# Kernel optimization log

Measured on AMD Instinct MI355X. Metric: run time of the kernel, lower is better.

The kernel has to match this reference:

```python
import jax, jax.numpy as jnp
import numpy as np

DIM = 512; H = 8; KH = 2; G = 4; DH = 64        # dim, q heads, kv heads, GQA group, head dim
BALL = 128; SEL = 64; TOPK = 2; PDIM = 3        # sliding ball, compress/selection block, topk, pos dim
SCALE = DH ** -0.5


def _rms_norm(x, gamma):
    return x * jax.lax.rsqrt(jnp.mean(x * x, axis=-1, keepdims=True) + 1e-6) * gamma


def _rotary(t):
    # t: (B, h, S, DH); GPT-NeoX style rotate-half rotary embedding
    S = t.shape[-2]
    inv = 1.0 / (10000.0 ** (jnp.arange(0, DH, 2, dtype=jnp.float32) / DH))
    f = jnp.arange(S, dtype=jnp.float32)[:, None] * inv          # (S, DH/2)
    cos = jnp.concatenate([jnp.cos(f), jnp.cos(f)], -1)
    sin = jnp.concatenate([jnp.sin(f), jnp.sin(f)], -1)
    t1, t2 = jnp.split(t, 2, -1)
    return t * cos + jnp.concatenate([-t2, t1], -1) * sin


def _forward(x, pos, pe_w, pe_b, gamma, wq, wk, wv, k_pos, v_pos,
             k_w1, k_b1, k_w2, k_b2, v_w1, v_b1, v_w2, v_b2,
             mem_k, mem_v, w_combine, w_out, num_batches):
    B = num_batches
    # relative position of leaves wrt ball center (no-grad in original)
    p = jax.lax.stop_gradient(pos).reshape(-1, SEL, PDIM)
    rel = (p - p.mean(axis=1, keepdims=True)).reshape(-1, PDIM)
    x = x + rel @ pe_w + pe_b
    x = x.reshape(B, -1, DIM)
    S = x.shape[1]
    nb = S // SEL
    h = _rms_norm(x, gamma)
    q = (h @ wq).reshape(B, S, H, DH).transpose(0, 2, 1, 3)      # (B,H,S,DH)
    k = (h @ wk).reshape(B, S, KH, DH).transpose(0, 2, 1, 3)     # (B,KH,S,DH)
    v = (h @ wv).reshape(B, S, KH, DH).transpose(0, 2, 1, 3)
    qr, kr = _rotary(q), _rotary(k)

    # --- compressed branch: per-block intra-pos emb + MLP compression ---
    kb = k.reshape(B, KH, nb, SEL, DH) + k_pos[None, :, None]
    vb = v.reshape(B, KH, nb, SEL, DH) + v_pos[None, :, None]
    ck = jax.nn.relu(kb.reshape(B, KH, nb, SEL * DH) @ k_w1 + k_b1) @ k_w2 + k_b2
    cv = jax.nn.relu(vb.reshape(B, KH, nb, SEL * DH) @ v_w1 + v_b1) @ v_w2 + v_b2
    ck = jnp.concatenate([jnp.broadcast_to(mem_k[None], (B, KH, 1, DH)), ck], axis=2)
    cv = jnp.concatenate([jnp.broadcast_to(mem_v[None], (B, KH, 1, DH)), cv], axis=2)
    qg = qr.reshape(B, KH, G, S, DH)
    csim = jnp.einsum('bkgsd,bknd->bkgsn', qg, ck) * SCALE
    cattn = jax.nn.softmax(csim, axis=-1)
    cout = jnp.einsum('bkgsn,bknd->bkgsd', cattn, cv).reshape(B, H, S, DH)

    # --- top-k block selection from compressed attention importance ---
    imp = cattn[..., 1:].mean(axis=2)                            # share over grouped q heads: (B,KH,S,nb)
    imp_blk = imp.reshape(B, KH, nb, SEL, nb).mean(axis=3)       # per query block: (B,KH,nb,nb)
    _, sel = jax.lax.top_k(imp_blk, TOPK)                        # (B,KH,nb,TOPK)

    # --- fine branch: each query block attends own + TOPK selected blocks ---
    kblk = kr.reshape(B, KH, nb, SEL, DH)
    vblk = v.reshape(B, KH, nb, SEL, DH)
    gather = jax.vmap(jax.vmap(lambda t, s: t[s]))               # (nb,SEL,DH),(nb,TOPK)->(nb,TOPK,SEL,DH)
    fk = jnp.concatenate([gather(kblk, sel), kblk[:, :, :, None]], axis=3)
    fv = jnp.concatenate([gather(vblk, sel), vblk[:, :, :, None]], axis=3)
    fk = fk.reshape(B, KH, nb, (TOPK + 1) * SEL, DH)
    fv = fv.reshape(B, KH, nb, (TOPK + 1) * SEL, DH)
    qb = qr.reshape(B, KH, G, nb, SEL, DH)
    fsim = jnp.einsum('bkgnqd,bknmd->bkgnqm', qb, fk) * SCALE
    fout = jnp.einsum('bkgnqm,bknmd->bkgnqd', jax.nn.softmax(fsim, -1), fv)
    fout = fout.reshape(B, H, S, DH)

    # --- sliding branch: MiniBallAttn = plain SDPA within balls of size 128 ---
    nw = S // BALL
    qw = qr.reshape(B, H, nw, BALL, DH)
    kw = jnp.repeat(kr, G, axis=1).reshape(B, H, nw, BALL, DH)
    vw = jnp.repeat(v, G, axis=1).reshape(B, H, nw, BALL, DH)
    ssim = jnp.einsum('bhnqd,bhnkd->bhnqk', qw, kw) * SCALE
    sout = jnp.einsum('bhnqk,bhnkd->bhnqd', jax.nn.softmax(ssim, -1), vw)
    sout = sout.reshape(B, H, S, DH)

    # --- sigmoid-gated strategy combine, merge heads, out projection ---
    gates = jax.nn.sigmoid(h @ w_combine).reshape(B, S, H, 3).transpose(0, 2, 1, 3)
    out = gates[..., 0:1] * cout + gates[..., 1:2] * fout + gates[..., 2:3] * sout
    out = out.transpose(0, 2, 1, 3).reshape(B, S, H * DH) @ w_out
    return out.reshape(-1, DIM)


def setup_inputs() -> dict:
    key = jax.random.key(0)
    ks = jax.random.split(key, 16)
    Bn, S = 8, 4096
    N = Bn * S
    CD = SEL * DH
    def lin(k, fi, fo):
        return (jax.random.normal(k, (fi, fo), jnp.float32) / np.sqrt(fi)).astype(jnp.float32)
    return {
        'x': jax.random.normal(ks[0], (N, DIM), jnp.float32),
        'pos': jax.random.normal(ks[1], (N, PDIM), jnp.float32),
        'pe_w': lin(ks[2], PDIM, DIM),
        'pe_b': jnp.zeros((DIM,), jnp.float32),
        'gamma': jnp.ones((DIM,), jnp.float32),
        'wq': lin(ks[3], DIM, H * DH),
        'wk': lin(ks[4], DIM, KH * DH),
        'wv': lin(ks[5], DIM, KH * DH),
        'k_pos': jax.random.normal(ks[6], (KH, SEL, DH), jnp.float32) * 0.02,
        'v_pos': jax.random.normal(ks[7], (KH, SEL, DH), jnp.float32) * 0.02,
        'k_w1': lin(ks[8], CD, CD), 'k_b1': jnp.zeros((CD,), jnp.float32),
        'k_w2': lin(ks[9], CD, DH), 'k_b2': jnp.zeros((DH,), jnp.float32),
        'v_w1': lin(ks[10], CD, CD), 'v_b1': jnp.zeros((CD,), jnp.float32),
        'v_w2': lin(ks[11], CD, DH), 'v_b2': jnp.zeros((DH,), jnp.float32),
        'mem_k': jax.random.normal(ks[12], (KH, 1, DH), jnp.float32) * 0.02,
        'mem_v': jax.random.normal(ks[13], (KH, 1, DH), jnp.float32) * 0.02,
        'w_combine': lin(ks[14], DIM, 3 * H),
        'w_out': lin(ks[15], H * DH, DIM),
        'num_batches': 8,
    }


def reference(x, pos, pe_w, pe_b, gamma, wq, wk, wv, k_pos, v_pos,
              k_w1, k_b1, k_w2, k_b2, v_w1, v_b1, v_w2, v_b2,
              mem_k, mem_v, w_combine, w_out, num_batches):
    return _forward(x, pos, pe_w, pe_b, gamma, wq, wk, wv, k_pos, v_pos,
                    k_w1, k_b1, k_w2, k_b2, v_w1, v_b1, v_w2, v_b2,
                    mem_k, mem_v, w_combine, w_out, num_batches)
```

## Files before the change

kernel.cpp:

```cpp
#include <hip/hip_runtime.h>
#include <stdint.h>

#define DEVI static __device__ __forceinline__
typedef unsigned short u16;
typedef __bf16 bhalf8 __attribute__((ext_vector_type(8)));
typedef float f32x4 __attribute__((ext_vector_type(4)));

DEVI u16 f2bf(float f) {
  union { float f; unsigned u; } v; v.f = f;
  unsigned r = v.u + 0x7FFFu + ((v.u >> 16) & 1u);
  return (u16)(r >> 16);
}
DEVI float bf2f(u16 h) {
  union { unsigned u; float f; } v; v.u = ((unsigned)h) << 16;
  return v.f;
}
DEVI f32x4 MFMA(bhalf8 a, bhalf8 b, f32x4 c) {
  return __builtin_amdgcn_mfma_f32_16x16x32_bf16(a, b, c, 0, 0, 0);
}
DEVI bhalf8 LD8(const u16* p) { return *(const bhalf8*)p; }
DEVI f32x4 zero4() { f32x4 z = {0.f, 0.f, 0.f, 0.f}; return z; }

#define GLDS16(gp, lp) __builtin_amdgcn_global_load_lds( \
    (const __attribute__((address_space(1))) void*)(gp), \
// ... 40 lines not shown
  if (bidx < 1792) {
    int idx = bidx * 256 + threadIdx.x;
    int k = idx & 511, n = idx >> 9;
    float v;
    if (n < 512) v = wq[(size_t)k*512 + n];
    else if (n < 640) v = wk[(size_t)k*128 + n - 512];
    else if (n < 768) v = wv[(size_t)k*128 + n - 640];
    else if (n < 792) v = wc[(size_t)k*24 + n - 768];
    else v = 0.f;
    u16 h = f2bf(v); hi[idx] = h; lo[idx] = f2bf(v - bf2f(h));
  } else {
    int idx = (bidx - 1792) * 256 + threadIdx.x;
    int s = idx >> 5, i = idx & 31;
    float e = (float)(2*i) * (1.0f/64.0f);
    float inv = 1.0f / powf(10000.0f, e);
    float f = (float)s * inv;
    ct[idx] = cosf(f); st[idx] = sinf(f);
  }
}

__global__ __launch_bounds__(256) void nsa_vT16(const u16* __restrict__ v16, u16* __restrict__ vT) {
  int blk = blockIdx.x;
  int st = (blk & 63) * 64, bkh = blk >> 6;
  __shared__ u16 tile[64][72];
  int t = threadIdx.x;
  int s = t >> 2, c0 = (t & 3) * 16;
  const u16* src = v16 + ((size_t)bkh*4096 + st + s) * 64;
  *(int4*)&tile[s][c0]   = *(const int4*)&src[c0];
  *(int4*)&tile[s][c0+8] = *(const int4*)&src[c0+8];
  __syncthreads();
  int d = t >> 2, s0 = (t & 3) * 16;
  u16* dst = vT + ((size_t)bkh*64 + d)*4096 + st + s0;
#pragma unroll
  for (int j = 0; j < 16; ++j) dst[j] = tile[s0+j][d];
}

__global__ __launch_bounds__(256) void nsa_wT(const float* __restrict__ src, u16* __restrict__ dhi,
    u16* __restrict__ dlo, int K, int N) {
  __shared__ float tile[64][65];
  int k0 = blockIdx.x * 64, n0 = blockIdx.y * 64;
  int t = threadIdx.x, r = t >> 2, c0 = (t & 3) * 16;
#pragma unroll
  for (int j = 0; j < 16; ++j) tile[r][c0+j] = src[(size_t)(k0+r)*N + n0 + c0 + j];
  __syncthreads();
  size_t ob = (size_t)(n0 + r)*K + k0 + c0;
#pragma unroll
  for (int j = 0; j < 16; ++j) {
    float v = tile[c0+j][r];
    u16 h = f2bf(v); dhi[ob+j] = h;
    if (dlo) dlo[ob+j] = f2bf(v - bf2f(h));
  }
}

__global__ __launch_bounds__(256) void nsa_init_c(const float* __restrict__ mem, const float* __restrict__ b2,
    float* __restrict__ c32) {
  int idx = blockIdx.x * 256 + threadIdx.x;
  if (idx >= 81920) return;
  int d = idx & 63, n = (idx >> 6) % 80, kh = (idx / (80*64)) & 1;
  c32[idx] = (n == 0) ? mem[kh*64 + d] : ((n <= 64) ? b2[d] : 0.f);
}

__global__ __launch_bounds__(256) void nsa_red64(const float* __restrict__ part, float* __restrict__ c32) {
  int idx = blockIdx.x * 256 + threadIdx.x;
  int m = idx >> 6, d = idx & 63;
  float s = 0.f;
#pragma unroll
  for (int kc = 0; kc < 8; ++kc) s += part[((size_t)kc*1024 + m)*64 + d];
  int bkh = m >> 6, n = m & 63;
  c32[(((size_t)bkh)*80 + 1 + n)*64 + d] += s;
}

template<bool SPLIT>
__global__ __launch_bounds__(256) void nsa_mlp_fuse(const float* __restrict__ part,
    const float* __restrict__ bias, u16* __restrict__ oh, u16* __restrict__ ol) {
  size_t i = ((size_t)blockIdx.x * 256 + threadIdx.x) * 4;
  int c = (int)(i & 4095);
  float4 a = *(const float4*)&part[i];
  float4 b = *(const float4*)&part[(size_t)4194304 + i];
  float v0 = fmaxf(a.x + b.x + bias[c+0], 0.f);
  float v1 = fmaxf(a.y + b.y + bias[c+1], 0.f);
  float v2 = fmaxf(a.z + b.z + bias[c+2], 0.f);
  float v3 = fmaxf(a.w + b.w + bias[c+3], 0.f);
  u16 h0 = f2bf(v0), h1 = f2bf(v1), h2 = f2bf(v2), h3 = f2bf(v3);
  ((unsigned long long*)oh)[i >> 2] = (unsigned long long)h0 | ((unsigned long long)h1 << 16) |
                                      ((unsigned long long)h2 << 32) | ((unsigned long long)h3 << 48);
  if (SPLIT) {
    u16 l0 = f2bf(v0 - bf2f(h0)), l1 = f2bf(v1 - bf2f(h1));
    u16 l2 = f2bf(v2 - bf2f(h2)), l3 = f2bf(v3 - bf2f(h3));
    ((unsigned long long*)ol)[i >> 2] = (unsigned long long)l0 | ((unsigned long long)l1 << 16) |
                                        ((unsigned long long)l2 << 32) | ((unsigned long long)l3 << 48);
  }
}

__global__ __launch_bounds__(256) void nsa_ckcv(const float* __restrict__ ck32, const float* __restrict__ cv32,
    u16* __restrict__ ckh, u16* __restrict__ ckl, u16* __restrict__ cvT) {
  int idx = blockIdx.x * 256 + threadIdx.x;
  if (idx < 81920) {
    float v = ck32[idx];
    u16 h = f2bf(v); ckh[idx] = h; ckl[idx] = f2bf(v - bf2f(h));
  } else if (idx < 81920 + 8*2*64*96) {
    int j = idx - 81920;
    int cc = j % 96, d = (j / 96) & 63, bkh = j / (96*64);
    float v = (cc < 80) ? cv32[((size_t)bkh*80 + cc)*64 + d] : 0.f;
    cvT[j] = f2bf(v);
  }
}

__global__ __launch_bounds__(256) void nsa_sentinel(float* __restrict__ o, int n, float val) {
  int i = blockIdx.x * 256 + threadIdx.x;
  if (i < n) o[i] = val;
}

template<bool SPLIT, int EPI>
__global__ __launch_bounds__(256) void nsa_gemm(const u16* __restrict__ Ah, const u16* __restrict__ Al,
    const u16* __restrict__ Bh, const u16* __restrict__ Bl, int K, int N,
    const float* __restrict__ p_cos, float* __restrict__ p_sin,
    u16* __restrict__ out_hi, u16* __restrict__ out_lo, float* __restrict__ og,
    const float* __restrict__ kpos, const float* __restrict__ vpos,
    u16* __restrict__ krb, u16* __restrict__ kbh, u16* __restrict__ kbl,
    u16* __restrict__ v16o, u16* __restrict__ vbh) {
  constexpr int NB = SPLIT ? 4 : 2;
  __shared__ u16 sm[NB * 2 * 4096];
  const int t = threadIdx.x, w = t >> 6, l = t & 63;
  const int wm = w >> 1, wn = w & 1;
  int m0, n0;
  if constexpr (EPI == 0) {
    const int bid = blockIdx.y * 256 + blockIdx.x;
    const int xcd = bid & 7, j = bid >> 3;
    const int mg = j / 56, rem = j % 56;
    const int nn = rem >> 3, mi = rem & 7;
    m0 = ((xcd * 4 + mg) * 8 + mi) * 128;
    n0 = nn * 128;
  } else {
    const int MBn = gridDim.x;
    const int nwg = MBn * gridDim.y;
    const int bid = blockIdx.y * MBn + blockIdx.x;
    const int swz = (bid & 7) * (nwg >> 3) + (bid >> 3);
    m0 = (swz % MBn) * 128; n0 = (swz / MBn) * 128;
  }
  const int klen = K / (int)gridDim.z;
  const int kb0 = blockIdx.z * klen;
  const int row = l & 15;
  const int kc8 = ((l >> 4) ^ ((l >> 1) & 3)) * 8;
  const int gsc = ((l & 3) ^ ((l >> 3) & 3)) * 8;
  const int sr = l >> 2;
  f32x4 acc[4][4];
#pragma unroll
  for (int a = 0; a < 4; ++a)
#pragma unroll
    for (int b = 0; b < 4; ++b) acc[a][b] = zero4();

  auto STAGE = [&](int buf, int k0) {
    u16* base = sm + buf * NB * 4096;
#pragma unroll
    for (int s2 = 0; s2 < 2; ++s2) {
      int seg = w*2 + s2;
      int r = seg*16 + sr;
      size_t ga = (size_t)(m0 + r)*K + k0 + gsc;
      size_t gb = (size_t)(n0 + r)*K + k0 + gsc;
      GLDS16(&Ah[ga], base + seg*512);
      GLDS16(&Bh[gb], base + 4096 + seg*512);
      if (SPLIT) {
        GLDS16(&Al[ga], base + 2*4096 + seg*512);
        GLDS16(&Bl[gb], base + 3*4096 + seg*512);
      }
    }
  };

  const int nt = klen >> 5;
  STAGE(0, kb0);
  __syncthreads();
  int cur = 0;
  for (int kt = 0; kt < nt; ++kt) {
    if (kt + 1 < nt) STAGE(cur ^ 1, kb0 + (kt + 1) * 32);
    u16* bA  = sm + cur * NB * 4096;
    u16* bB  = bA + 4096;
    u16* bAl = bA + 2*4096;
    u16* bBl = bA + 3*4096;
    bhalf8 af[4], afl[4];
#pragma unroll
    for (int mf = 0; mf < 4; ++mf) {
      af[mf] = LD8(&bA[(wm*64 + mf*16 + row)*32 + kc8]);
      if (SPLIT) afl[mf] = LD8(&bAl[(wm*64 + mf*16 + row)*32 + kc8]);
    }
#pragma unroll
// ... 96 lines not shown
#pragma unroll
    for (int mf = 0; mf < 4; ++mf)
#pragma unroll
      for (int nf = 0; nf < 4; ++nf)
#pragma unroll
        for (int i = 0; i < 4; ++i) {
          int r = m0 + wm*64 + mf*16 + (l >> 4)*4 + i;
          int c = n0 + wn*64 + nf*16 + (l & 15);
          p_sin[(size_t)r*N + c] = acc[mf][nf][i];
        }
  } else {
    const int M = (int)gridDim.x * 128;
#pragma unroll
    for (int mf = 0; mf < 4; ++mf)
#pragma unroll
      for (int nf = 0; nf < 4; ++nf)
#pragma unroll
        for (int i = 0; i < 4; ++i) {
          int r = m0 + wm*64 + mf*16 + (l >> 4)*4 + i;
          int c = n0 + wn*64 + nf*16 + (l & 15);
          p_sin[((size_t)blockIdx.z * M + r) * (size_t)N + c] = acc[mf][nf][i];
        }
  }
}

template<bool SPLIT>
__global__ __launch_bounds__(256) void nsa_gemm64(const u16* __restrict__ Ah, const u16* __restrict__ Al,
    const u16* __restrict__ Bh, const u16* __restrict__ Bl, float* __restrict__ part) {
  constexpr int NB = SPLIT ? 4 : 2;
  __shared__ u16 sm[NB * 2 * 2048];
  const int t = threadIdx.x, w = t >> 6, l = t & 63;
  const int mt = blockIdx.x, kc = blockIdx.y;
  const int row = l & 15;
  const int kc8 = ((l >> 4) ^ ((l >> 1) & 3)) * 8;
  const int gsc = ((l & 3) ^ ((l >> 3) & 3)) * 8;
  const int sr = l >> 2;
  f32x4 acc[4];
#pragma unroll
  for (int a = 0; a < 4; ++a) acc[a] = zero4();

  auto STAGE = [&](int buf, int k0) {
    u16* base = sm + buf * NB * 2048;
    int r = w*16 + sr;
    size_t ga = (size_t)(mt*64 + r)*4096 + k0 + gsc;
    size_t gb = (size_t)r*4096 + k0 + gsc;
    GLDS16(&Ah[ga], base + w*512);
    GLDS16(&Bh[gb], base + 2048 + w*512);
    if (SPLIT) {
      GLDS16(&Al[ga], base + 2*2048 + w*512);
      GLDS16(&Bl[gb], base + 3*2048 + w*512);
    }
  };

  STAGE(0, kc*512);
  __syncthreads();
  int cur = 0;
  for (int kt = 0; kt < 16; ++kt) {
    if (kt + 1 < 16) STAGE(cur ^ 1, kc*512 + (kt + 1) * 32);
    u16* bA  = sm + cur * NB * 2048;
    u16* bB  = bA + 2048;
    u16* bAl = bA + 2*2048;
    u16* bBl = bA + 3*2048;
    bhalf8 a = LD8(&bA[(w*16 + row)*32 + kc8]);
    bhalf8 al;
    if (SPLIT) al = LD8(&bAl[(w*16 + row)*32 + kc8]);
#pragma unroll
    for (int nf = 0; nf < 4; ++nf) {
      bhalf8 b = LD8(&bB[(nf*16 + row)*32 + kc8]);
      bhalf8 bl;
      if (SPLIT) bl = LD8(&bBl[(nf*16 + row)*32 + kc8]);
      acc[nf] = MFMA(a, b, acc[nf]);
      if (SPLIT) {
        acc[nf] = MFMA(a, bl, acc[nf]);
        acc[nf] = MFMA(al, b, acc[nf]);
      }
    }
    __syncthreads();
    cur ^= 1;
  }
#pragma unroll
  for (int nf = 0; nf < 4; ++nf)
#pragma unroll
    for (int i = 0; i < 4; ++i) {
      int m = mt*64 + w*16 + (l >> 4)*4 + i;
      int d = nf*16 + (l & 15);
      part[((size_t)kc*1024 + m)*64 + d] = acc[nf][i];
    }
}


__global__ __launch_bounds__(256) void nsa_attn_comp(const u16* __restrict__ qrh, const u16* __restrict__ qrl,
    const u16* __restrict__ ckh, const u16* __restrict__ ckl, const u16* __restrict__ cvT,
    const float* __restrict__ g32, u16* __restrict__ comb, float* __restrict__ imp) {
  __shared__ u16 smem[27392];
  __shared__ float sImp[4 * 80];
  u16* sKh = smem;
  u16* sKl = smem + 5760;
  u16* sVT = smem + 11520;
  u16* sQh = smem + 18176;
  u16* sQl = smem + 22784;
  u16* sP  = smem + 18176;
  const int t = threadIdx.x, w = t >> 6, l = t & 63;
  const int bid = blockIdx.x;
  const int qt = bid & 63, kh = (bid >> 6) & 1, b = bid >> 7;
  const int row = l & 15, kg = (l >> 4) * 8;
  size_t kbase = (size_t)(b*2 + kh) * 80 * 64;
  size_t vbase = (size_t)(b*2 + kh) * 64 * 96;
  for (int e = t; e < 640; e += 256) {
    int r = e >> 3, c = (e & 7) * 8;
    *(int4*)&sKh[r*72 + c] = *(const int4*)&ckh[kbase + r*64 + c];
    *(int4*)&sKl[r*72 + c] = *(const int4*)&ckl[kbase + r*64 + c];
  }
  for (int e = t; e < 768; e += 256) {
    int r = e / 12, ch = e % 12;
    *(int4*)&sVT[r*104 + ch*8] = *(const int4*)&cvT[vbase + (size_t)r*96 + ch*8];
  }
  float accImp = 0.f;
  for (int g = 0; g < 4; ++g) {
    if (g) __syncthreads();
    size_t qbase = ((size_t)((b*2 + kh)*4 + g)*4096 + qt*64) * 64;
    for (int e = t; e < 512; e += 256) {
      int r = e >> 3, c = (e & 7) * 8;
      *(int4*)&sQh[r*72 + c] = *(const int4*)&qrh[qbase + r*64 + c];
      *(int4*)&sQl[r*72 + c] = *(const int4*)&qrl[qbase + r*64 + c];
    }
    __syncthreads();
    f32x4 sc[5];
#pragma unroll
    for (int nf = 0; nf < 5; ++nf) sc[nf] = zero4();
#pragma unroll
    for (int kk = 0; kk < 2; ++kk) {
      bhalf8 ah = LD8(&sQh[(w*16 + row)*72 + kk*32 + kg]);
      bhalf8 al = LD8(&sQl[(w*16 + row)*72 + kk*32 + kg]);
#pragma unroll
      for (int nf = 0; nf < 5; ++nf) {
        bhalf8 bh = LD8(&sKh[(nf*16 + row)*72 + kk*32 + kg]);
        bhalf8 bl = LD8(&sKl[(nf*16 + row)*72 + kk*32 + kg]);
        sc[nf] = MFMA(ah, bh, sc[nf]);
        sc[nf] = MFMA(ah, bl, sc[nf]);
        sc[nf] = MFMA(al, bh, sc[nf]);
      }
    }
    float mx[4] = {-1e30f, -1e30f, -1e30f, -1e30f};
#pragma unroll
    for (int nf = 0; nf < 5; ++nf)
#pragma unroll
      for (int i = 0; i < 4; ++i) {
        int col = nf*16 + (l & 15);
        float v = (col < 65) ? sc[nf][i] * 0.125f : -1e30f;
        sc[nf][i] = v;
        mx[i] = fmaxf(mx[i], v);
      }
#pragma unroll
    for (int i = 0; i < 4; ++i)
#pragma unroll
      for (int o = 1; o < 16; o <<= 1) mx[i] = fmaxf(mx[i], __shfl_xor(mx[i], o));
    float sum[4] = {0.f, 0.f, 0.f, 0.f};
#pragma unroll
    for (int nf = 0; nf < 5; ++nf)
#pragma unroll
      for (int i = 0; i < 4; ++i) {
        int col = nf*16 + (l & 15);
        float p = (col < 65) ? expf(sc[nf][i] - mx[i]) : 0.f;
        sc[nf][i] = p;
        sum[i] += p;
      }
#pragma unroll
    for (int i = 0; i < 4; ++i)
#pragma unroll
      for (int o = 1; o < 16; o <<= 1) sum[i] += __shfl_xor(sum[i], o);
    float inv[4];
#pragma unroll
    for (int i = 0; i < 4; ++i) inv[i] = 1.0f / sum[i];
    __syncthreads();
#pragma unroll
    for (int nf = 0; nf < 5; ++nf)
#pragma unroll
      for (int i = 0; i < 4; ++i)
        sP[(w*16 + (l >> 4)*4 + i)*104 + nf*16 + (l & 15)] = f2bf(sc[nf][i] * inv[i]);
#pragma unroll
    for (int i = 0; i < 4; ++i)
      sP[(w*16 + (l >> 4)*4 + i)*104 + 80 + (l & 15)] = 0;
#pragma unroll
    for (int nf = 0; nf < 5; ++nf) {
      float cs = 0.f;
#pragma unroll
      for (int i = 0; i < 4; ++i) cs += sc[nf][i] * inv[i];
      cs += __shfl_xor(cs, 16);
      cs += __shfl_xor(cs, 32);
      if (l < 16) sImp[w*80 + nf*16 + l] = cs;
    }
    __syncthreads();
    if (t < 64) {
      int n = t + 1;
      accImp += sImp[n] + sImp[80 + n] + sImp[160 + n] + sImp[240 + n];
    }
    f32x4 ov[4];
#pragma unroll
    for (int nf = 0; nf < 4; ++nf) ov[nf] = zero4();
#pragma unroll
    for (int kk = 0; kk < 3; ++kk) {
      bhalf8 a = LD8(&sP[(w*16 + row)*104 + kk*32 + kg]);
#pragma unroll
      for (int nf = 0; nf < 4; ++nf) {
        bhalf8 bv = LD8(&sVT[(nf*16 + row)*104 + kk*32 + kg]);
        ov[nf] = MFMA(a, bv, ov[nf]);
      }
    }
    int hq = kh*4 + g;
#pragma unroll
    for (int i = 0; i < 4; ++i) {
      int q = qt*64 + w*16 + (l >> 4)*4 + i;
      float gate = g32[((size_t)b*4096 + q)*24 + hq*3 + 0];
#pragma unroll
      for (int nf = 0; nf < 4; ++nf) {
        int d = nf*16 + (l & 15);
        comb[(((size_t)b*4096 + q)*8 + hq)*64 + d] = f2bf(gate * ov[nf][i]);
      }
    }
  }
  if (t < 64) imp[(size_t)bid*64 + t] = accImp * (1.0f/256.0f);
}

__global__ __launch_bounds__(64) void nsa_top2(const float* __restrict__ imp, int* __restrict__ sel) {
  int blk = blockIdx.x;
  int l = threadIdx.x;
  float v = imp[(size_t)blk*64 + l];
  float v1 = v; int i1 = l;
#pragma unroll
  for (int o = 1; o < 64; o <<= 1) {
    float ovv = __shfl_xor(v1, o); int oi = __shfl_xor(i1, o);
    if (ovv > v1 || (ovv == v1 && oi < i1)) { v1 = ovv; i1 = oi; }
  }
  float v2 = (l == i1) ? -3.0e38f : v; int i2 = l;
#pragma unroll
  for (int o = 1; o < 64; o <<= 1) {
    float ovv = __shfl_xor(v2, o); int oi = __shfl_xor(i2, o);
    if (ovv > v2 || (ovv == v2 && oi < i2)) { v2 = ovv; i2 = oi; }
  }
  if (l == 0) { sel[blk*2 + 0] = i1; sel[blk*2 + 1] = i2; }
}

__global__ __launch_bounds__(256) void nsa_attn_fine(const u16* __restrict__ qrh, const u16* __restrict__ kr,
    const u16* __restrict__ vT, const int* __restrict__ sel, const float* __restrict__ g32,
    u16* __restrict__ comb) {
  __shared__ u16 smem[31232];
  u16* sK  = smem;
  u16* sP  = smem;
  u16* sVT = smem + 13824;
  u16* sQ  = smem + 26624;
  const int t = threadIdx.x, w = t >> 6, l = t & 63;
  const int bid = blockIdx.x;
  const int qt = bid & 63, kh = (bid >> 6) & 1, b = bid >> 7;
  const int row = l & 15, kg = (l >> 4) * 8;
  const int s0 = sel[bid*2 + 0] & 63, s1 = sel[bid*2 + 1] & 63;
  size_t kvb = (size_t)(b*2 + kh) * 4096 * 64;
  size_t vtb = (size_t)(b*2 + kh) * 64 * 4096;
  for (int e = t; e < 1536; e += 256) {
    int r = e / 24, ch = e % 24;
    int n0 = ch * 8, bi = n0 >> 6;
    int blkid = (bi == 0) ? s0 : ((bi == 1) ? s1 : qt);
    int sidx = blkid*64 + (n0 & 63);
    *(int4*)&sVT[r*200 + n0] = *(const int4*)&vT[vtb + (size_t)r*4096 + sidx];
  }
  for (int g = 0; g < 4; ++g) {
    __syncthreads();
    for (int e = t; e < 1536; e += 256) {
      int r = e >> 3, c = (e & 7) * 8;
      int bi = r >> 6;
      int blkid = (bi == 0) ? s0 : ((bi == 1) ? s1 : qt);
      int sidx = blkid*64 + (r & 63);
      *(int4*)&sK[r*72 + c] = *(const int4*)&kr[kvb + (size_t)sidx*64 + c];
    }
    size_t qbase = ((size_t)((b*2 + kh)*4 + g)*4096 + qt*64) * 64;
    for (int e = t; e < 512; e += 256) {
      int r = e >> 3, c = (e & 7) * 8;
      *(int4*)&sQ[r*72 + c] = *(const int4*)&qrh[qbase + r*64 + c];
    }
    __syncthreads();
    f32x4 sc[12];
#pragma unroll
    for (int nf = 0; nf < 12; ++nf) sc[nf] = zero4();
#pragma unroll
    for (int kk = 0; kk < 2; ++kk) {
      bhalf8 a = LD8(&sQ[(w*16 + row)*72 + kk*32 + kg]);
#pragma unroll
      for (int nf = 0; nf < 12; ++nf) {
        bhalf8 bk = LD8(&sK[(nf*16 + row)*72 + kk*32 + kg]);
        sc[nf] = MFMA(a, bk, sc[nf]);
      }
    }
    float mx[4] = {-1e30f, -1e30f, -1e30f, -1e30f};
#pragma unroll
    for (int nf = 0; nf < 12; ++nf)
#pragma unroll
      for (int i = 0; i < 4; ++i) {
        float v = sc[nf][i] * 0.125f;
        sc[nf][i] = v;
        mx[i] = fmaxf(mx[i], v);
      }
#pragma unroll
    for (int i = 0; i < 4; ++i)
#pragma unroll
      for (int o = 1; o < 16; o <<= 1) mx[i] = fmaxf(mx[i], __shfl_xor(mx[i], o));
    float sum[4] = {0.f, 0.f, 0.f, 0.f};
#pragma unroll
    for (int nf = 0; nf < 12; ++nf)
#pragma unroll
      for (int i = 0; i < 4; ++i) {
        float p = expf(sc[nf][i] - mx[i]);
        sc[nf][i] = p;
        sum[i] += p;
      }
#pragma unroll
    for (int i = 0; i < 4; ++i)
#pragma unroll
      for (int o = 1; o < 16; o <<= 1) sum[i] += __shfl_xor(sum[i], o);
    float inv[4];
#pragma unroll
    for (int i = 0; i < 4; ++i) inv[i] = 1.0f / sum[i];
    __syncthreads();
#pragma unroll
    for (int nf = 0; nf < 12; ++nf)
#pragma unroll
      for (int i = 0; i < 4; ++i)
        sP[(w*16 + (l >> 4)*4 + i)*200 + nf*16 + (l & 15)] = f2bf(sc[nf][i] * inv[i]);
    __syncthreads();
    f32x4 ovv[4];
#pragma unroll
    for (int nf = 0; nf < 4; ++nf) ovv[nf] = zero4();
#pragma unroll
    for (int kk = 0; kk < 6; ++kk) {
      bhalf8 a = LD8(&sP[(w*16 + row)*200 + kk*32 + kg]);
#pragma unroll
      for (int nf = 0; nf < 4; ++nf) {
        bhalf8 bv = LD8(&sVT[(nf*16 + row)*200 + kk*32 + kg]);
        ovv[nf] = MFMA(a, bv, ovv[nf]);
      }
    }
    int hq = kh*4 + g;
#pragma unroll
    for (int i = 0; i < 4; ++i) {
      int q = qt*64 + w*16 + (l >> 4)*4 + i;
      float gate = g32[((size_t)b*4096 + q)*24 + hq*3 + 1];
#pragma unroll
      for (int nf = 0; nf < 4; ++nf) {
        int d = nf*16 + (l & 15);
        size_t oi = (((size_t)b*4096 + q)*8 + hq)*64 + d;
        comb[oi] = f2bf(bf2f(comb[oi]) + gate * ovv[nf][i]);
      }
    }
  }
}

__global__ __launch_bounds__(256) void nsa_attn_slide(const u16* __restrict__ qrh, const u16* __restrict__ kr,
    const u16* __restrict__ vT, const float* __restrict__ g32, u16* __restrict__ comb) {
  __shared__ u16 smem[31232];
  u16* sK  = smem;
  u16* sVT = smem + 9216;
  u16* sQ  = smem + 17920;
  u16* sP  = smem + 22528;
  const int t = threadIdx.x, w = t >> 6, l = t & 63;
  const int bid = blockIdx.x;
  const int ball = bid & 31, kh = (bid >> 5) & 1, b = bid >> 6;
  const int row = l & 15, kg = (l >> 4) * 8;
  const int ks0 = ball * 128;
  size_t kvb = (size_t)(b*2 + kh) * 4096 * 64;
  size_t vtb = (size_t)(b*2 + kh) * 64 * 4096;
  for (int e = t; e < 1024; e += 256) {
    int r = e >> 3, c = (e & 7) * 8;
    *(int4*)&sK[r*72 + c] = *(const int4*)&kr[kvb + (size_t)(ks0 + r)*64 + c];
  }
  for (int e = t; e < 1024; e += 256) {
    int r = e >> 4, ch = e & 15;
    *(int4*)&sVT[r*136 + ch*8] = *(const int4*)&vT[vtb + (size_t)r*4096 + ks0 + ch*8];
  }
  for (int hq = 0; hq < 4; ++hq) {
    int hh = kh*4 + hq;
    for (int qh = 0; qh < 2; ++qh) {
      int qt = ball*2 + qh;
      __syncthreads();
      size_t qbase = ((size_t)(b*8 + hh)*4096 + qt*64) * 64;
      for (int e = t; e < 512; e += 256) {
        int r = e >> 3, c = (e & 7) * 8;
        *(int4*)&sQ[r*72 + c] = *(const int4*)&qrh[qbase + r*64 + c];
      }
      __syncthreads();
      f32x4 sc[8];
#pragma unroll
      for (int nf = 0; nf < 8; ++nf) sc[nf] = zero4();
#pragma unroll
      for (int kk = 0; kk < 2; ++kk) {
        bhalf8 a = LD8(&sQ[(w*16 + row)*72 + kk*32 + kg]);
#pragma unroll
        for (int nf = 0; nf < 8; ++nf) {
          bhalf8 bk = LD8(&sK[(nf*16 + row)*72 + kk*32 + kg]);
          sc[nf] = MFMA(a, bk, sc[nf]);
        }
      }
      float mx[4] = {-1e30f, -1e30f, -1e30f, -1e30f};
#pragma unroll
      for (int nf = 0; nf < 8; ++nf)
#pragma unroll
        for (int i = 0; i < 4; ++i) {
          float v = sc[nf][i] * 0.125f;
          sc[nf][i] = v;
          mx[i] = fmaxf(mx[i], v);
        }
#pragma unroll
      for (int i = 0; i < 4; ++i)
#pragma unroll
        for (int o = 1; o < 16; o <<= 1) mx[i] = fmaxf(mx[i], __shfl_xor(mx[i], o));
      float sum[4] = {0.f, 0.f, 0.f, 0.f};
#pragma unroll
      for (int nf = 0; nf < 8; ++nf)
#pragma unroll
        for (int i = 0; i < 4; ++i) {
          float p = expf(sc[nf][i] - mx[i]);
          sc[nf][i] = p;
          sum[i] += p;
        }
#pragma unroll
      for (int i = 0; i < 4; ++i)
#pragma unroll
        for (int o = 1; o < 16; o <<= 1) sum[i] += __shfl_xor(sum[i], o);
      float inv[4];
#pragma unroll
      for (int i = 0; i < 4; ++i) inv[i] = 1.0f / sum[i];
#pragma unroll
      for (int nf = 0; nf < 8; ++nf)
#pragma unroll
        for (int i = 0; i < 4; ++i)
          sP[(w*16 + (l >> 4)*4 + i)*136 + nf*16 + (l & 15)] = f2bf(sc[nf][i] * inv[i]);
      f32x4 ovv[4];
#pragma unroll
      for (int nf = 0; nf < 4; ++nf) ovv[nf] = zero4();
#pragma unroll
      for (int kk = 0; kk < 4; ++kk) {
        bhalf8 a = LD8(&sP[(w*16 + row)*136 + kk*32 + kg]);
#pragma unroll
        for (int nf = 0; nf < 4; ++nf) {
          bhalf8 bv = LD8(&sVT[(nf*16 + row)*136 + kk*32 + kg]);
          ovv[nf] = MFMA(a, bv, ovv[nf]);
        }
      }
#pragma unroll
// ... 1 lines not shown
        int q = qt*64 + w*16 + (l >> 4)*4 + i;
        float gate = g32[((size_t)b*4096 + q)*24 + hh*3 + 2];
#pragma unroll
        for (int nf = 0; nf < 4; ++nf) {
          int d = nf*16 + (l & 15);
          size_t oi = (((size_t)b*4096 + q)*8 + hh)*64 + d;
          comb[oi] = f2bf(bf2f(comb[oi]) + gate * ovv[nf][i]);
        }
      }
    }
  }
}


extern "C" void kernel_launch(void* const* d_in, const int* in_sizes, int n_in,
                              void* d_out, int out_size, void* d_ws, size_t ws_size,
                              hipStream_t stream) {
  const float* x     = (const float*)d_in[0];
  const float* pos   = (const float*)d_in[1];
  const float* pe_w  = (const float*)d_in[2];
  const float* pe_b  = (const float*)d_in[3];
  const float* gamma = (const float*)d_in[4];
  const float* wq    = (const float*)d_in[5];
  const float* wk    = (const float*)d_in[6];
  const float* wv    = (const float*)d_in[7];
  const float* k_pos = (const float*)d_in[8];
  const float* v_pos = (const float*)d_in[9];
  const float* k_w1  = (const float*)d_in[10];
  const float* k_b1  = (const float*)d_in[11];
  const float* k_w2  = (const float*)d_in[12];
  const float* k_b2  = (const float*)d_in[13];
  const float* v_w1  = (const float*)d_in[14];
  const float* v_b1  = (const float*)d_in[15];
  const float* v_w2  = (const float*)d_in[16];
  const float* v_b2  = (const float*)d_in[17];
  const float* mem_k = (const float*)d_in[18];
  const float* mem_v = (const float*)d_in[19];
  const float* w_cmb = (const float*)d_in[20];
  const float* w_out = (const float*)d_in[21];
  float* out = (float*)d_out;
  char* ws = (char*)d_ws;

  size_t off = 0;
  auto A = [&](size_t b) { size_t o = off; off += (b + 255) & ~(size_t)255; return o; };
  const size_t oR1 = A(67108864);
  const size_t oR2 = A(67108864);
  const size_t oR4 = A(16777216);
  const size_t oR5 = A(16777216);
  const size_t oR6 = A(16777216);
  const size_t oR7 = A(16777216);
  const size_t oR8 = A(3145728);
  const size_t oR9 = A(2097152);
  const size_t o_cos = A(524288),  o_sin = A(524288);
  const size_t o_ck32 = A(327680), o_cv32 = A(327680);
  const size_t o_ckh = A(163840),  o_ckl = A(163840);
  const size_t o_cvT = A(196608);
  const size_t o_woh = A(524288),  o_wol = A(524288);
  const size_t o_imp = A(262144);
  const size_t o_sel = A(8192);
  const size_t o_part = A(2097152);
  const size_t o_part1 = A(33554432);

  if (ws_size < off) {
    nsa_sentinel<<<(out_size + 255)/256, 256, 0, stream>>>(out, out_size, (float)(ws_size >> 20));
    return;
  }

#define WP(T, o) ((T*)(ws + (o)))
  u16*  h_hi = WP(u16, oR1);           u16* h_lo = WP(u16, oR1 + 33554432);
  u16*  w1h  = WP(u16, oR1);           u16* w1l  = WP(u16, oR1 + 33554432);
  u16*  combp = WP(u16, oR1);
  u16*  qrh  = WP(u16, oR2);           u16* qrl  = WP(u16, oR2 + 33554432);
  u16*  th   = WP(u16, oR4);           u16* tl   = WP(u16, oR4 + 8388608);
  u16*  v16b = WP(u16, oR5);           u16* vbh  = WP(u16, oR5 + 8388608);
  u16*  kbh  = WP(u16, oR6);           u16* kbl  = WP(u16, oR6 + 8388608);
  u16*  krb  = WP(u16, oR7);           u16* vTb  = WP(u16, oR7 + 8388608);
  float* g32 = WP(float, oR8);
  u16*  wch  = WP(u16, oR9);           u16* wcl  = WP(u16, oR9 + 917504);
  u16*  w2h  = WP(u16, oR9);           u16* w2l  = WP(u16, oR9 + 524288);
  u16*  w2vh = WP(u16, oR9 + 1048576); u16* w2vl = WP(u16, oR9 + 1572864);
  float* cosb = WP(float, o_cos);      float* sinb = WP(float, o_sin);
  float* ck32 = WP(float, o_ck32);     float* cv32 = WP(float, o_cv32);
  u16*  ckh  = WP(u16, o_ckh);         u16* ckl  = WP(u16, o_ckl);
  u16*  cvT  = WP(u16, o_cvT);
  u16*  woh  = WP(u16, o_woh);         u16* wol  = WP(u16, o_wol);
  float* imp = WP(float, o_imp);
  int*  selp = WP(int, o_sel);
  float* part = WP(float, o_part);
  float* part1 = WP(float, o_part1);

  nsa_hnorm<<<32768, 256, 0, stream>>>(x, pos, pe_w, pe_b, gamma, h_hi, h_lo);
  nsa_wcat_rope<<<2304, 256, 0, stream>>>(wq, wk, wv, w_cmb, wch, wcl, cosb, sinb);
  nsa_gemm<true, 0><<<dim3(256, 7, 1), 256, 0, stream>>>(h_hi, h_lo, wch, wcl, 512, 896,
      cosb, sinb, qrh, qrl, g32, k_pos, v_pos, krb, kbh, kbl, v16b, vbh);
  nsa_vT16<<<1024, 256, 0, stream>>>(v16b, vTb);
  nsa_wT<<<dim3(64, 64), 256, 0, stream>>>(k_w1, w1h, w1l, 4096, 4096);
  nsa_gemm<true, 3><<<dim3(8, 32, 2), 256, 0, stream>>>(kbh, kbl, w1h, w1l, 4096, 4096,
      nullptr, part1, nullptr, nullptr, nullptr, nullptr, nullptr, nullptr, nullptr, nullptr,
      nullptr, nullptr);
  nsa_mlp_fuse<true><<<4096, 256, 0, stream>>>(part1, k_b1, th, tl);
  nsa_wT<<<dim3(64, 1), 256, 0, stream>>>(k_w2, w2h, w2l, 4096, 64);
  nsa_init_c<<<320, 256, 0, stream>>>(mem_k, k_b2, ck32);
  nsa_gemm64<true><<<dim3(16, 8), 256, 0, stream>>>(th, tl, w2h, w2l, part);
  nsa_red64<<<256, 256, 0, stream>>>(part, ck32);
  nsa_wT<<<dim3(64, 64), 256, 0, stream>>>(v_w1, w1h, nullptr, 4096, 4096);
  nsa_gemm<false, 3><<<dim3(8, 32, 2), 256, 0, stream>>>(vbh, nullptr, w1h, nullptr, 4096, 4096,
      nullptr, part1, nullptr, nullptr, nullptr, nullptr, nullptr, nullptr, nullptr, nullptr,
      nullptr, nullptr);
  nsa_mlp_fuse<false><<<4096, 256, 0, stream>>>(part1, v_b1, th, nullptr);
  nsa_wT<<<dim3(64, 1), 256, 0, stream>>>(v_w2, w2vh, nullptr, 4096, 64);
  nsa_init_c<<<320, 256, 0, stream>>>(mem_v, v_b2, cv32);
  nsa_gemm64<false><<<dim3(16, 8), 256, 0, stream>>>(th, nullptr, w2vh, nullptr, part);
  nsa_red64<<<256, 256, 0, stream>>>(part, cv32);
  nsa_ckcv<<<704, 256, 0, stream>>>(ck32, cv32, ckh, ckl, cvT);
  nsa_attn_comp<<<1024, 256, 0, stream>>>(qrh, qrl, ckh, ckl, cvT, g32, combp, imp);
  nsa_top2<<<1024, 64, 0, stream>>>(imp, selp);
  nsa_attn_fine<<<1024, 256, 0, stream>>>(qrh, krb, vTb, selp, g32, combp);
  nsa_attn_slide<<<512, 256, 0, stream>>>(qrh, krb, vTb, g32, combp);
  nsa_wT<<<dim3(8, 8), 256, 0, stream>>>(w_out, woh, nullptr, 512, 512);
  nsa_gemm<false, 2><<<dim3(256, 4, 1), 256, 0, stream>>>(combp, nullptr, woh, nullptr, 512, 512,
      nullptr, out, nullptr, nullptr, nullptr, nullptr, nullptr, nullptr, nullptr, nullptr,
      nullptr, nullptr);
#undef WP
}
```

Baseline: 703.3 us.

## Fuse compression reductions, split QKV gemm precision, load Q directly to registers

Merges init, reduction and bf16 conversion of the compressed K/V into single kernels, removing the fp32 staging buffers and three launches. It doubles the split-K factor of the 64-wide gemm. The QKV projection is split so the columns after the first five tiles run without the hi/lo split-precision path. The attention kernels load Q straight from global memory into registers instead of staging it in LDS, and the fine kernel loads K once rather than per group, which removes several barriers per iteration. Dropping the split precision on those columns may lower their accuracy, and taking sP out of the K region grows the fine kernel's LDS use.

```diff
diff --git a/kernel.cpp b/kernel.cpp
--- a/kernel.cpp
+++ b/kernel.cpp
@@ -116,22 +116,38 @@
   }
 }
 
-__global__ __launch_bounds__(256) void nsa_init_c(const float* __restrict__ mem, const float* __restrict__ b2,
-    float* __restrict__ c32) {
+__global__ __launch_bounds__(256) void nsa_red_ck(const float* __restrict__ part, const float* __restrict__ mem,
+    const float* __restrict__ b2, u16* __restrict__ ckh, u16* __restrict__ ckl) {
   int idx = blockIdx.x * 256 + threadIdx.x;
   if (idx >= 81920) return;
-  int d = idx & 63, n = (idx >> 6) % 80, kh = (idx / (80*64)) & 1;
-  c32[idx] = (n == 0) ? mem[kh*64 + d] : ((n <= 64) ? b2[d] : 0.f);
-}
-
-__global__ __launch_bounds__(256) void nsa_red64(const float* __restrict__ part, float* __restrict__ c32) {
+  int d = idx & 63, n = (idx >> 6) % 80, bkh = idx / (80*64);
+  int kh = bkh & 1;
+  float v;
+  if (n == 0) v = mem[kh*64 + d];
+  else if (n <= 64) {
+    v = b2[d];
+    int m = bkh*64 + (n - 1);
+#pragma unroll
+    for (int kc = 0; kc < 16; ++kc) v += part[((size_t)kc*1024 + m)*64 + d];
+  } else v = 0.f;
+  u16 h = f2bf(v); ckh[idx] = h; ckl[idx] = f2bf(v - bf2f(h));
+}
+
+__global__ __launch_bounds__(256) void nsa_red_cv(const float* __restrict__ part, const float* __restrict__ mem,
+    const float* __restrict__ b2, u16* __restrict__ cvT) {
   int idx = blockIdx.x * 256 + threadIdx.x;
-  int m = idx >> 6, d = idx & 63;
-  float s = 0.f;
-#pragma unroll
-  for (int kc = 0; kc < 8; ++kc) s += part[((size_t)kc*1024 + m)*64 + d];
-  int bkh = m >> 6, n = m & 63;
-  c32[(((size_t)bkh)*80 + 1 + n)*64 + d] += s;
+  if (idx >= 98304) return;
+  int cc = idx % 96, d = (idx / 96) & 63, bkh = idx / (96*64);
+  int kh = bkh & 1;
+  float v;
+  if (cc == 0) v = mem[kh*64 + d];
+  else if (cc <= 64) {
+    v = b2[d];
+    int m = bkh*64 + (cc - 1);
+#pragma unroll
+    for (int kc = 0; kc < 16; ++kc) v += part[((size_t)kc*1024 + m)*64 + d];
+  } else v = 0.f;
+  cvT[idx] = f2bf(v);
 }
 
 template<bool SPLIT>
@@ -156,26 +172,12 @@
   }
 }
 
-__global__ __launch_bounds__(256) void nsa_ckcv(const float* __restrict__ ck32, const float* __restrict__ cv32,
-    u16* __restrict__ ckh, u16* __restrict__ ckl, u16* __restrict__ cvT) {
-  int idx = blockIdx.x * 256 + threadIdx.x;
-  if (idx < 81920) {
-    float v = ck32[idx];
-    u16 h = f2bf(v); ckh[idx] = h; ckl[idx] = f2bf(v - bf2f(h));
-  } else if (idx < 81920 + 8*2*64*96) {
-    int j = idx - 81920;
-    int cc = j % 96, d = (j / 96) & 63, bkh = j / (96*64);
-    float v = (cc < 80) ? cv32[((size_t)bkh*80 + cc)*64 + d] : 0.f;
-    cvT[j] = f2bf(v);
-  }
-}
-
 __global__ __launch_bounds__(256) void nsa_sentinel(float* __restrict__ o, int n, float val) {
   int i = blockIdx.x * 256 + threadIdx.x;
   if (i < n) o[i] = val;
 }
 
-template<bool SPLIT, int EPI>
+template<bool SPLIT, int EPI, int NOFF = 0>
 __global__ __launch_bounds__(256) void nsa_gemm(const u16* __restrict__ Ah, const u16* __restrict__ Al,
     const u16* __restrict__ Bh, const u16* __restrict__ Bl, int K, int N,
     const float* __restrict__ p_cos, float* __restrict__ p_sin,
@@ -189,12 +191,13 @@
   const int wm = w >> 1, wn = w & 1;
   int m0, n0;
   if constexpr (EPI == 0) {
+    const int nper = (int)gridDim.y;
     const int bid = blockIdx.y * 256 + blockIdx.x;
     const int xcd = bid & 7, j = bid >> 3;
-    const int mg = j / 56, rem = j % 56;
+    const int mg = j / (8*nper), rem = j % (8*nper);
     const int nn = rem >> 3, mi = rem & 7;
     m0 = ((xcd * 4 + mg) * 8 + mi) * 128;
-    n0 = nn * 128;
+    n0 = (nn + NOFF) * 128;
   } else {
     const int MBn = gridDim.x;
     const int nwg = MBn * gridDim.y;
@@ -397,11 +400,11 @@
     }
   };
 
-  STAGE(0, kc*512);
+  STAGE(0, kc*256);
   __syncthreads();
   int cur = 0;
-  for (int kt = 0; kt < 16; ++kt) {
-    if (kt + 1 < 16) STAGE(cur ^ 1, kc*512 + (kt + 1) * 32);
+  for (int kt = 0; kt < 8; ++kt) {
+    if (kt + 1 < 8) STAGE(cur ^ 1, kc*256 + (kt + 1) * 32);
     u16* bA  = sm + cur * NB * 2048;
     u16* bB  = bA + 2048;
     u16* bAl = bA + 2*2048;
@@ -437,13 +440,11 @@
 __global__ __launch_bounds__(256) void nsa_attn_comp(const u16* __restrict__ qrh, const u16* __restrict__ qrl,
     const u16* __restrict__ ckh, const u16* __restrict__ ckl, const u16* __restrict__ cvT,
     const float* __restrict__ g32, u16* __restrict__ comb, float* __restrict__ imp) {
-  __shared__ u16 smem[27392];
+  __shared__ u16 smem[24832];
   __shared__ float sImp[4 * 80];
   u16* sKh = smem;
   u16* sKl = smem + 5760;
   u16* sVT = smem + 11520;
-  u16* sQh = smem + 18176;
-  u16* sQl = smem + 22784;
   u16* sP  = smem + 18176;
   const int t = threadIdx.x, w = t >> 6, l = t & 63;
   const int bid = blockIdx.x;
@@ -460,23 +461,24 @@
     int r = e / 12, ch = e % 12;
     *(int4*)&sVT[r*104 + ch*8] = *(const int4*)&cvT[vbase + (size_t)r*96 + ch*8];
   }
-  float accImp = 0.f;
+  for (int e = l; e < 80; e += 64) sImp[w*80 + e] = 0.f;
+#pragma unroll
+  for (int i = 0; i < 4; ++i)
+    sP[(w*16 + (l & 15))*104 + 80 + (l >> 4)*4 + i] = 0;
+  __syncthreads();
   for (int g = 0; g < 4; ++g) {
-    if (g) __syncthreads();
-    size_t qbase = ((size_t)((b*2 + kh)*4 + g)*4096 + qt*64) * 64;
-    for (int e = t; e < 512; e += 256) {
-      int r = e >> 3, c = (e & 7) * 8;
-      *(int4*)&sQh[r*72 + c] = *(const int4*)&qrh[qbase + r*64 + c];
-      *(int4*)&sQl[r*72 + c] = *(const int4*)&qrl[qbase + r*64 + c];
-    }
-    __syncthreads();
+    size_t qbase = ((size_t)((b*2 + kh)*4 + g)*4096 + qt*64) * 64 + (size_t)(w*16 + row)*64;
+    bhalf8 ah0 = LD8(&qrh[qbase + kg]);
+    bhalf8 ah1 = LD8(&qrh[qbase + 32 + kg]);
+    bhalf8 al0 = LD8(&qrl[qbase + kg]);
+    bhalf8 al1 = LD8(&qrl[qbase + 32 + kg]);
     f32x4 sc[5];
 #pragma unroll
     for (int nf = 0; nf < 5; ++nf) sc[nf] = zero4();
 #pragma unroll
     for (int kk = 0; kk < 2; ++kk) {
-      bhalf8 ah = LD8(&sQh[(w*16 + row)*72 + kk*32 + kg]);
-      bhalf8 al = LD8(&sQl[(w*16 + row)*72 + kk*32 + kg]);
+      bhalf8 ah = kk ? ah1 : ah0;
+      bhalf8 al = kk ? al1 : al0;
 #pragma unroll
       for (int nf = 0; nf < 5; ++nf) {
         bhalf8 bh = LD8(&sKh[(nf*16 + row)*72 + kk*32 + kg]);
@@ -517,15 +519,11 @@
     float inv[4];
 #pragma unroll
     for (int i = 0; i < 4; ++i) inv[i] = 1.0f / sum[i];
-    __syncthreads();
 #pragma unroll
     for (int nf = 0; nf < 5; ++nf)
 #pragma unroll
       for (int i = 0; i < 4; ++i)
         sP[(w*16 + (l >> 4)*4 + i)*104 + nf*16 + (l & 15)] = f2bf(sc[nf][i] * inv[i]);
-#pragma unroll
-    for (int i = 0; i < 4; ++i)
-      sP[(w*16 + (l >> 4)*4 + i)*104 + 80 + (l & 15)] = 0;
 #pragma unroll
     for (int nf = 0; nf < 5; ++nf) {
       float cs = 0.f;
@@ -533,12 +531,7 @@
       for (int i = 0; i < 4; ++i) cs += sc[nf][i] * inv[i];
       cs += __shfl_xor(cs, 16);
       cs += __shfl_xor(cs, 32);
-      if (l < 16) sImp[w*80 + nf*16 + l] = cs;
-    }
-    __syncthreads();
-    if (t < 64) {
-      int n = t + 1;
-      accImp += sImp[n] + sImp[80 + n] + sImp[160 + n] + sImp[240 + n];
+      if (l < 16) sImp[w*80 + nf*16 + l] += cs;
     }
     f32x4 ov[4];
 #pragma unroll
@@ -564,7 +557,11 @@
       }
     }
   }
-  if (t < 64) imp[(size_t)bid*64 + t] = accImp * (1.0f/256.0f);
+  __syncthreads();
+  if (t < 64) {
+    int n = t + 1;
+    imp[(size_t)bid*64 + t] = (sImp[n] + sImp[80 + n] + sImp[160 + n] + sImp[240 + n]) * (1.0f/256.0f);
+  }
 }
 
 __global__ __launch_bounds__(64) void nsa_top2(const float* __restrict__ imp, int* __restrict__ sel) {
@@ -589,11 +586,10 @@
 __global__ __launch_bounds__(256) void nsa_attn_fine(const u16* __restrict__ qrh, const u16* __restrict__ kr,
     const u16* __restrict__ vT, const int* __restrict__ sel, const float* __restrict__ g32,
     u16* __restrict__ comb) {
-  __shared__ u16 smem[31232];
+  __shared__ u16 smem[39424];
   u16* sK  = smem;
-  u16* sP  = smem;
   u16* sVT = smem + 13824;
-  u16* sQ  = smem + 26624;
+  u16* sP  = smem + 26624;
   const int t = threadIdx.x, w = t >> 6, l = t & 63;
   const int bid = blockIdx.x;
   const int qt = bid & 63, kh = (bid >> 6) & 1, b = bid >> 7;
@@ -602,33 +598,30 @@
   size_t kvb = (size_t)(b*2 + kh) * 4096 * 64;
   size_t vtb = (size_t)(b*2 + kh) * 64 * 4096;
   for (int e = t; e < 1536; e += 256) {
+    int r = e >> 3, c = (e & 7) * 8;
+    int bi = r >> 6;
+    int blkid = (bi == 0) ? s0 : ((bi == 1) ? s1 : qt);
+    int sidx = blkid*64 + (r & 63);
+    *(int4*)&sK[r*72 + c] = *(const int4*)&kr[kvb + (size_t)sidx*64 + c];
+  }
+  for (int e = t; e < 1536; e += 256) {
     int r = e / 24, ch = e % 24;
     int n0 = ch * 8, bi = n0 >> 6;
     int blkid = (bi == 0) ? s0 : ((bi == 1) ? s1 : qt);
     int sidx = blkid*64 + (n0 & 63);
     *(int4*)&sVT[r*200 + n0] = *(const int4*)&vT[vtb + (size_t)r*4096 + sidx];
   }
+  __syncthreads();
   for (int g = 0; g < 4; ++g) {
-    __syncthreads();
-    for (int e = t; e < 1536; e += 256) {
-      int r = e >> 3, c = (e & 7) * 8;
-      int bi = r >> 6;
-      int blkid = (bi == 0) ? s0 : ((bi == 1) ? s1 : qt);
-      int sidx = blkid*64 + (r & 63);
-      *(int4*)&sK[r*72 + c] = *(const int4*)&kr[kvb + (size_t)sidx*64 + c];
-    }
-    size_t qbase = ((size_t)((b*2 + kh)*4 + g)*4096 + qt*64) * 64;
-    for (int e = t; e < 512; e += 256) {
-      int r = e >> 3, c = (e & 7) * 8;
-      *(int4*)&sQ[r*72 + c] = *(const int4*)&qrh[qbase + r*64 + c];
-    }
-    __syncthreads();
+    size_t qbase = ((size_t)((b*2 + kh)*4 + g)*4096 + qt*64) * 64 + (size_t)(w*16 + row)*64;
+    bhalf8 a0 = LD8(&qrh[qbase + kg]);
+    bhalf8 a1 = LD8(&qrh[qbase + 32 + kg]);
     f32x4 sc[12];
 #pragma unroll
     for (int nf = 0; nf < 12; ++nf) sc[nf] = zero4();
 #pragma unroll
     for (int kk = 0; kk < 2; ++kk) {
-      bhalf8 a = LD8(&sQ[(w*16 + row)*72 + kk*32 + kg]);
+      bhalf8 a = kk ? a1 : a0;
 #pragma unroll
       for (int nf = 0; nf < 12; ++nf) {
         bhalf8 bk = LD8(&sK[(nf*16 + row)*72 + kk*32 + kg]);
@@ -664,13 +657,11 @@
     float inv[4];
 #pragma unroll
     for (int i = 0; i < 4; ++i) inv[i] = 1.0f / sum[i];
-    __syncthreads();
 #pragma unroll
     for (int nf = 0; nf < 12; ++nf)
 #pragma unroll
       for (int i = 0; i < 4; ++i)
         sP[(w*16 + (l >> 4)*4 + i)*200 + nf*16 + (l & 15)] = f2bf(sc[nf][i] * inv[i]);
-    __syncthreads();
     f32x4 ovv[4];
 #pragma unroll
     for (int nf = 0; nf < 4; ++nf) ovv[nf] = zero4();
@@ -700,11 +691,10 @@
 
 __global__ __launch_bounds__(256) void nsa_attn_slide(const u16* __restrict__ qrh, const u16* __restrict__ kr,
     const u16* __restrict__ vT, const float* __restrict__ g32, u16* __restrict__ comb) {
-  __shared__ u16 smem[31232];
+  __shared__ u16 smem[26624];
   u16* sK  = smem;
   u16* sVT = smem + 9216;
-  u16* sQ  = smem + 17920;
-  u16* sP  = smem + 22528;
+  u16* sP  = smem + 17920;
   const int t = threadIdx.x, w = t >> 6, l = t & 63;
   const int bid = blockIdx.x;
   const int ball = bid & 31, kh = (bid >> 5) & 1, b = bid >> 6;
@@ -720,23 +710,20 @@
     int r = e >> 4, ch = e & 15;
     *(int4*)&sVT[r*136 + ch*8] = *(const int4*)&vT[vtb + (size_t)r*4096 + ks0 + ch*8];
   }
+  __syncthreads();
   for (int hq = 0; hq < 4; ++hq) {
     int hh = kh*4 + hq;
     for (int qh = 0; qh < 2; ++qh) {
       int qt = ball*2 + qh;
-      __syncthreads();
-      size_t qbase = ((size_t)(b*8 + hh)*4096 + qt*64) * 64;
-      for (int e = t; e < 512; e += 256) {
-        int r = e >> 3, c = (e & 7) * 8;
-        *(int4*)&sQ[r*72 + c] = *(const int4*)&qrh[qbase + r*64 + c];
-      }
-      __syncthreads();
+      size_t qbase = ((size_t)(b*8 + hh)*4096 + qt*64) * 64 + (size_t)(w*16 + row)*64;
+      bhalf8 a0 = LD8(&qrh[qbase + kg]);
+      bhalf8 a1 = LD8(&qrh[qbase + 32 + kg]);
       f32x4 sc[8];
 #pragma unroll
       for (int nf = 0; nf < 8; ++nf) sc[nf] = zero4();
 #pragma unroll
       for (int kk = 0; kk < 2; ++kk) {
-        bhalf8 a = LD8(&sQ[(w*16 + row)*72 + kk*32 + kg]);
+        bhalf8 a = kk ? a1 : a0;
 #pragma unroll
         for (int nf = 0; nf < 8; ++nf) {
           bhalf8 bk = LD8(&sK[(nf*16 + row)*72 + kk*32 + kg]);
@@ -844,13 +831,12 @@
   const size_t oR8 = A(3145728);
   const size_t oR9 = A(2097152);
   const size_t o_cos = A(524288),  o_sin = A(524288);
-  const size_t o_ck32 = A(327680), o_cv32 = A(327680);
   const size_t o_ckh = A(163840),  o_ckl = A(163840);
   const size_t o_cvT = A(196608);
   const size_t o_woh = A(524288),  o_wol = A(524288);
   const size_t o_imp = A(262144);
   const size_t o_sel = A(8192);
-  const size_t o_part = A(2097152);
+  const size_t o_part = A(4194304);
   const size_t o_part1 = A(33554432);
 
   if (ws_size < off) {
@@ -872,7 +858,6 @@
   u16*  w2h  = WP(u16, oR9);           u16* w2l  = WP(u16, oR9 + 524288);
   u16*  w2vh = WP(u16, oR9 + 1048576); u16* w2vl = WP(u16, oR9 + 1572864);
   float* cosb = WP(float, o_cos);      float* sinb = WP(float, o_sin);
-  float* ck32 = WP(float, o_ck32);     float* cv32 = WP(float, o_cv32);
   u16*  ckh  = WP(u16, o_ckh);         u16* ckl  = WP(u16, o_ckl);
   u16*  cvT  = WP(u16, o_cvT);
   u16*  woh  = WP(u16, o_woh);         u16* wol  = WP(u16, o_wol);
@@ -883,7 +868,9 @@
 
   nsa_hnorm<<<32768, 256, 0, stream>>>(x, pos, pe_w, pe_b, gamma, h_hi, h_lo);
   nsa_wcat_rope<<<2304, 256, 0, stream>>>(wq, wk, wv, w_cmb, wch, wcl, cosb, sinb);
-  nsa_gemm<true, 0><<<dim3(256, 7, 1), 256, 0, stream>>>(h_hi, h_lo, wch, wcl, 512, 896,
+  nsa_gemm<true, 0, 0><<<dim3(256, 5, 1), 256, 0, stream>>>(h_hi, h_lo, wch, wcl, 512, 896,
+      cosb, sinb, qrh, qrl, g32, k_pos, v_pos, krb, kbh, kbl, v16b, vbh);
+  nsa_gemm<false, 0, 5><<<dim3(256, 2, 1), 256, 0, stream>>>(h_hi, nullptr, wch, nullptr, 512, 896,
       cosb, sinb, qrh, qrl, g32, k_pos, v_pos, krb, kbh, kbl, v16b, vbh);
   nsa_vT16<<<1024, 256, 0, stream>>>(v16b, vTb);
   nsa_wT<<<dim3(64, 64), 256, 0, stream>>>(k_w1, w1h, w1l, 4096, 4096);
@@ -892,19 +879,16 @@
       nullptr, nullptr);
   nsa_mlp_fuse<true><<<4096, 256, 0, stream>>>(part1, k_b1, th, tl);
   nsa_wT<<<dim3(64, 1), 256, 0, stream>>>(k_w2, w2h, w2l, 4096, 64);
-  nsa_init_c<<<320, 256, 0, stream>>>(mem_k, k_b2, ck32);
-  nsa_gemm64<true><<<dim3(16, 8), 256, 0, stream>>>(th, tl, w2h, w2l, part);
-  nsa_red64<<<256, 256, 0, stream>>>(part, ck32);
+  nsa_gemm64<true><<<dim3(16, 16), 256, 0, stream>>>(th, tl, w2h, w2l, part);
+  nsa_red_ck<<<320, 256, 0, stream>>>(part, mem_k, k_b2, ckh, ckl);
   nsa_wT<<<dim3(64, 64), 256, 0, stream>>>(v_w1, w1h, nullptr, 4096, 4096);
   nsa_gemm<false, 3><<<dim3(8, 32, 2), 256, 0, stream>>>(vbh, nullptr, w1h, nullptr, 4096, 4096,
       nullptr, part1, nullptr, nullptr, nullptr, nullptr, nullptr, nullptr, nullptr, nullptr,
       nullptr, nullptr);
   nsa_mlp_fuse<false><<<4096, 256, 0, stream>>>(part1, v_b1, th, nullptr);
   nsa_wT<<<dim3(64, 1), 256, 0, stream>>>(v_w2, w2vh, nullptr, 4096, 64);
-  nsa_init_c<<<320, 256, 0, stream>>>(mem_v, v_b2, cv32);
-  nsa_gemm64<false><<<dim3(16, 8), 256, 0, stream>>>(th, nullptr, w2vh, nullptr, part);
-  nsa_red64<<<256, 256, 0, stream>>>(part, cv32);
-  nsa_ckcv<<<704, 256, 0, stream>>>(ck32, cv32, ckh, ckl, cvT);
+  nsa_gemm64<false><<<dim3(16, 16), 256, 0, stream>>>(th, nullptr, w2vh, nullptr, part);
+  nsa_red_cv<<<384, 256, 0, stream>>>(part, mem_v, v_b2, cvT);
   nsa_attn_comp<<<1024, 256, 0, stream>>>(qrh, qrl, ckh, ckl, cvT, g32, combp, imp);
   nsa_top2<<<1024, 64, 0, stream>>>(imp, selp);
   nsa_attn_fine<<<1024, 256, 0, stream>>>(qrh, krb, vTb, selp, g32, combp);
```

Result: slower. 723.6 us (+2.9%).
